# Kernel tuning notes

Measured on AMD Instinct MI355X. Metric: run time of the kernel, lower is better.

The kernel has to match this reference:

```python
import jax, jax.numpy as jnp
import numpy as np

N = 512
NODE_IN = 64
NODE_OUT = 64
ED_IN = 32
ED_OUT = 32
STATE = 80  # must satisfy 2*NODE_IN + ED_IN == 2*STATE
SLOPE = 0.1
EPS = 1e-5


def setup_inputs() -> dict:
    key = jax.random.key(0)
    ks = jax.random.split(key, 10)
    def lin(k, out_f, in_f):
        return jax.random.normal(k, (out_f, in_f), jnp.float32) / np.sqrt(in_f).astype(np.float32)
    x = jax.random.normal(ks[0], (N, NODE_IN), jnp.float32)
    edge_attr = jax.random.normal(ks[1], (N * N, ED_IN), jnp.float32)
    mask = jax.random.randint(ks[2], (N * N, 1), 0, 2).astype(jnp.int32)
    return {
        "x": x,
        "edge_attr": edge_attr,
        "mask": mask,
        "W_nu": lin(ks[3], NODE_OUT, NODE_IN),
        "b_nu": jnp.zeros((NODE_OUT,), jnp.float32),
        "W_h2": lin(ks[4], STATE, 2 * STATE),
        "b_h2": jnp.zeros((STATE,), jnp.float32),
        "W_eo": lin(ks[5], ED_OUT, STATE),
        "b_eo": jnp.zeros((ED_OUT,), jnp.float32),
        "e_vec": jax.random.normal(ks[6], (2 * NODE_OUT + ED_OUT,), jnp.float32) * 0.1,
        "bn_n_w": jnp.ones((NODE_OUT,), jnp.float32),
        "bn_n_b": jnp.zeros((NODE_OUT,), jnp.float32),
        "bn_e_w": jnp.ones((ED_OUT,), jnp.float32),
        "bn_e_b": jnp.zeros((ED_OUT,), jnp.float32),
    }


def _lrelu(v):
    return jax.nn.leaky_relu(v, SLOPE)


def _bn(v, w, b):
    # BatchNorm1d, training-mode (batch stats, biased variance)
    mu = v.mean(axis=0)
    var = v.var(axis=0)
    return (v - mu) / jnp.sqrt(var + EPS) * w + b


def reference(x, edge_attr, mask, W_nu, b_nu, W_h2, b_h2, W_eo, b_eo, e_vec,
              bn_n_w, bn_n_b, bn_e_w, bn_e_b):
    n = x.shape[0]
    m = mask.astype(x.dtype)  # [N*N, 1]
    # triplet_e[i*N+j] = [x_i, edge_attr_{ij}, x_j]
    src = jnp.repeat(x, n, axis=0)          # [N*N, NODE_IN]
    dst = jnp.tile(x, (n, 1))               # [N*N, NODE_IN]
    triplet_e = jnp.concatenate([src, edge_attr, dst], axis=-1)  # [N*N, 2*STATE]
    # NOTE: ed_trans_layer / ed_hidden_1 outputs are dead code in the source.
    h = _lrelu(triplet_e @ W_h2.T + b_h2)                 # [N*N, STATE]
    new_edge_attr = _lrelu(h @ W_eo.T + b_eo)             # [N*N, ED_OUT]
    new_edge_attr = new_edge_attr * m
    xn = _lrelu(x @ W_nu.T + b_nu)                        # [N, NODE_OUT]
    triplet_n = jnp.concatenate(
        [jnp.repeat(xn, n, axis=0), new_edge_attr, jnp.tile(xn, (n, 1))], axis=-1
    ).reshape(n, n, 2 * NODE_OUT + ED_OUT)
    scores = _lrelu(jnp.einsum("ijd,d->ij", triplet_n, e_vec))  # [N, N]
    att = jax.nn.softmax(scores, axis=1)
    att = (att.reshape(n * n, 1) * m).reshape(n, n)
    # dropout disabled (deterministic / eval)
    new_x = att @ xn                                       # [N, NODE_OUT]
    new_x = _bn(new_x, bn_n_w, bn_n_b)
    new_edge_attr = _bn(new_edge_attr, bn_e_w, bn_e_b)
    return new_x, new_edge_attr
```

## Files before the change

kernel.cpp:

```cpp
#include <hip/hip_runtime.h>

#define SLOPE 0.1f
#define EPS 1e-5f

typedef __bf16 bf16x8 __attribute__((ext_vector_type(8)));
typedef unsigned short u16x8 __attribute__((ext_vector_type(8)));
typedef float f32x4 __attribute__((ext_vector_type(4)));

#define WS_ESUM 0
#define WS_ESQ 32
#define WS_A 192
#define WS_B 704
#define WS_XN 1216
#define WS_NEWX 33984
#define WS_P1B 66752
#define WS_P2 107712
#define WS_SC 148672
#define WSH_WB 821632
#define WSH_WO 826752

__device__ __forceinline__ float lrelu(float v) { return v > 0.f ? v : SLOPE * v; }
__device__ __forceinline__ unsigned short f2bf(float f) {
  unsigned x = __float_as_uint(f);
  return (unsigned short)((x + 0x7fffu + ((x >> 16) & 1u)) >> 16);
}

__global__ void __launch_bounds__(256) k1(const float* __restrict__ x,
                                          const float* __restrict__ W_nu,
                                          const float* __restrict__ b_nu,
                                          const float* __restrict__ W_h2,
                                          const float* __restrict__ b_h2,
                                          const float* __restrict__ W_eo,
                                          const float* __restrict__ ev,
                                          float* ws, float* __restrict__ part) {
  int blk = blockIdx.x;
  int tid = threadIdx.x;
  unsigned short* wsh = (unsigned short*)ws;
  if (blk < 128) {
    __shared__ float wlds[64 * 65];
#pragma unroll
    for (int it = 0; it < 16; it++) {
      int idx = it * 256 + tid;
      wlds[(idx >> 6) * 65 + (idx & 63)] = W_nu[idx];
    }
    int gid = blk * 256 + tid;
    part[gid] = 0.f;
    if (gid < 5120) {
      wsh[WSH_WB + gid] = f2bf(W_h2[(gid >> 6) * 160 + 64 + (gid & 63)]);
    } else if (gid < 8192) {
      int idx = gid - 5120;
      int n = idx / 96, kk = idx - 96 * n;
      wsh[WSH_WO + idx] = (kk < 80) ? f2bf(W_eo[n * 80 + kk]) : (unsigned short)0;
    }
    __syncthreads();
    int i = blk * 4 + (tid >> 6);
    int c = tid & 63;
    float acc = b_nu[c];
    const float* xr = x + i * 64;
#pragma unroll 8
    for (int k = 0; k < 64; k++) acc += xr[k] * wlds[c * 65 + k];
    float xnv = lrelu(acc);
    ws[WS_XN + i * 64 + c] = xnv;
    float va = xnv * ev[c];
    float vb = xnv * ev[96 + c];
#pragma unroll
    for (int off = 32; off >= 1; off >>= 1) {
      va += __shfl_xor(va, off, 64);
      vb += __shfl_xor(vb, off, 64);
    }
    if (c == 0) { ws[WS_A + i] = va; ws[WS_B + i] = vb; }
  } else {
    int b2 = blk - 128;
    int bm = b2 & 7, bn = b2 >> 3;
    int wave = tid >> 6, lane = tid & 63;
    int c16 = lane & 15, q = lane >> 4;
    int n = bn * 16 + c16;
    const float* wrow = (n < 80) ? (W_h2 + n * 160) : (W_h2 + (n - 80) * 160 + 96);
    int mrow = bm * 64 + wave * 16 + c16;
    bf16x8 bf[2], af[2];
#pragma unroll
    for (int ks = 0; ks < 2; ks++) {
      const float* bs = wrow + ks * 32 + q * 8;
      const float* as = x + mrow * 64 + ks * 32 + q * 8;
      u16x8 ub, ua;
#pragma unroll
      for (int jj = 0; jj < 8; jj++) { ub[jj] = f2bf(bs[jj]); ua[jj] = f2bf(as[jj]); }
      bf[ks] = __builtin_bit_cast(bf16x8, ub);
      af[ks] = __builtin_bit_cast(bf16x8, ua);
    }
    float bias = (n < 80) ? b_h2[n] : 0.f;
    f32x4 acc = {bias, bias, bias, bias};
    acc = __builtin_amdgcn_mfma_f32_16x16x32_bf16(af[0], bf[0], acc, 0, 0, 0);
    acc = __builtin_amdgcn_mfma_f32_16x16x32_bf16(af[1], bf[1], acc, 0, 0, 0);
#pragma unroll
    for (int r = 0; r < 4; r++) {
      int mm = bm * 64 + wave * 16 + q * 4 + r;
      if (n < 80) ws[WS_P1B + mm * 80 + n] = acc[r];
      else        ws[WS_P2 + mm * 80 + (n - 80)] = acc[r];
    }
  }
}

__global__ void __launch_bounds__(256) k2(const float* __restrict__ ea,
                                          const int* __restrict__ mask,
                                          const float* __restrict__ b_eo,
                                          const float* __restrict__ ev,
                                          float* ws,
                                          float* __restrict__ part,
                                          float* __restrict__ out_e) {
  __shared__ unsigned short ht[64 * 104];
  __shared__ float wred[2][4][32];
  int tid = threadIdx.x;
  int wave = tid >> 6, lane = tid & 63;
  int c16 = lane & 15, q = lane >> 4;
  int blk = blockIdx.x;
  int i = blk >> 3, j0 = (blk & 7) << 6;
  const unsigned short* wsh = (const unsigned short*)ws;

  bf16x8 wb[5];
#pragma unroll
  for (int t = 0; t < 5; t++)
    wb[t] = __builtin_bit_cast(
        bf16x8, *(const u16x8*)(wsh + WSH_WB + (t * 16 + c16) * 64 + q * 8));
  int mA = i * 512 + j0 + wave * 16 + c16;
  bf16x8 af;
  {
    const float* src = ea + mA * 32 + q * 8;
    u16x8 u;
#pragma unroll
    for (int jj = 0; jj < 8; jj++) u[jj] = f2bf(src[jj]);
    af = __builtin_bit_cast(bf16x8, u);
  }

  f32x4 acc[5];
#pragma unroll
  for (int t = 0; t < 5; t++) {
    int n = t * 16 + c16;
    float p1v = ws[WS_P1B + i * 80 + n];
#pragma unroll
    for (int r = 0; r < 4; r++) {
      int j = j0 + wave * 16 + q * 4 + r;
      acc[t][r] = p1v + ws[WS_P2 + j * 80 + n];
    }
  }
#pragma unroll
  for (int t = 0; t < 5; t++)
    acc[t] = __builtin_amdgcn_mfma_f32_16x16x32_bf16(af, wb[t], acc[t], 0, 0, 0);

#pragma unroll
  for (int t = 0; t < 5; t++)
#pragma unroll
    for (int r = 0; r < 4; r++)
      ht[(wave * 16 + q * 4 + r) * 104 + t * 16 + c16] = f2bf(lrelu(acc[t][r]));

  bf16x8 wo[2][3];
#pragma unroll
  for (int t2 = 0; t2 < 2; t2++)
#pragma unroll
    for (int s = 0; s < 3; s++)
      wo[t2][s] = __builtin_bit_cast(
          bf16x8,
          *(const u16x8*)(wsh + WSH_WO + (t2 * 16 + c16) * 96 + s * 32 + q * 8));

  f32x4 z4 = {0.f, 0.f, 0.f, 0.f};
  f32x4 acc2[2] = {z4, z4};
  int hrow = wave * 16 + c16;
#pragma unroll
  for (int s = 0; s < 3; s++) {
    int kk = s * 32 + q * 8;
    u16x8 hbits = {0, 0, 0, 0, 0, 0, 0, 0};
    if (kk < 80) hbits = *(const u16x8*)&ht[hrow * 104 + kk];
    bf16x8 ha = __builtin_bit_cast(bf16x8, hbits);
#pragma unroll
    for (int t2 = 0; t2 < 2; t2++)
      acc2[t2] = __builtin_amdgcn_mfma_f32_16x16x32_bf16(ha, wo[t2][s], acc2[t2], 0, 0, 0);
  }

  float beo[2] = {b_eo[c16], b_eo[16 + c16]};
  float eve[2] = {ev[64 + c16], ev[80 + c16]};
  float ne[2][4];
  float scs[2] = {0.f, 0.f}, scss[2] = {0.f, 0.f};
#pragma unroll
  for (int t2 = 0; t2 < 2; t2++)
#pragma unroll
    for (int r = 0; r < 4; r++) {
      int m = i * 512 + j0 + wave * 16 + q * 4 + r;
      float mf = mask[m] ? 1.f : 0.f;
      float v = lrelu(acc2[t2][r] + beo[t2]) * mf;
      ne[t2][r] = v;
      scs[t2] += v;
      scss[t2] += v * v;
      out_e[m * 32 + t2 * 16 + c16] = v;
    }
#pragma unroll
  for (int t2 = 0; t2 < 2; t2++) {
    float a_ = scs[t2], b_ = scss[t2];
    a_ += __shfl_xor(a_, 16, 64); a_ += __shfl_xor(a_, 32, 64);
    b_ += __shfl_xor(b_, 16, 64); b_ += __shfl_xor(b_, 32, 64);
    if (q == 0) {
      wred[0][wave][t2 * 16 + c16] = a_;
      wred[1][wave][t2 * 16 + c16] = b_;
    }
  }
  float se[4];
#pragma unroll
  for (int r = 0; r < 4; r++) {
    float s = ne[0][r] * eve[0] + ne[1][r] * eve[1];
#pragma unroll
    for (int off = 8; off >= 1; off >>= 1) s += __shfl_xor(s, off, 64);
    se[r] = s;
  }
  if (c16 < 4) {
    float s = (c16 == 0) ? se[0] : (c16 == 1) ? se[1] : (c16 == 2) ? se[2] : se[3];
    int j = j0 + wave * 16 + q * 4 + c16;
    ws[WS_SC + i * 512 + j] = lrelu(ws[WS_A + i] + ws[WS_B + j] + s);
  }
  __syncthreads();
  if (tid < 64) {
    int half = tid >> 5;
    int col = tid & 31;
    float v = wred[half][0][col] + wred[half][1][col] + wred[half][2][col] +
              wred[half][3][col];
    atomicAdd(&part[(blk >> 3) * 64 + tid], v);
  }
}

__global__ void __launch_bounds__(512) k3(const int* __restrict__ mask,
                                          const float* __restrict__ part,
                                          float* ws) {
  __shared__ float att[512];
  __shared__ float red[8];
  __shared__ float nx[8][64];
  int i = blockIdx.x, tid = threadIdx.x;
  int wave = tid >> 6, lane = tid & 63;
  if (i == 512) {
    int c = tid & 63, g = tid >> 6;
    float a = 0.f;
    for (int s = g; s < 512; s += 8) a += part[s * 64 + c];
    nx[g][c] = a;
    __syncthreads();
    if (tid < 64) {
      float t = 0.f;
#pragma unroll
      for (int g2 = 0; g2 < 8; g2++) t += nx[g2][tid];
      ws[WS_ESUM + tid] = t;
    }
    return;
  }
  float p = __expf(ws[WS_SC + i * 512 + tid]);
  float sm = p;
#pragma unroll
  for (int off = 32; off >= 1; off >>= 1) sm += __shfl_xor(sm, off, 64);
  if (lane == 0) red[wave] = sm;
  __syncthreads();
  float tot = red[0] + red[1] + red[2] + red[3] + red[4] + red[5] + red[6] + red[7];
  att[tid] = p * (1.f / tot) * (mask[i * 512 + tid] ? 1.f : 0.f);
  __syncthreads();
  int c = lane;
  const float* xn = ws + WS_XN;
  float accv = 0.f;
#pragma unroll 4
  for (int u = 0; u < 64; u++) {
    int j = wave * 64 + u;
    accv += att[j] * xn[j * 64 + c];
  }
  nx[wave][c] = accv;
  __syncthreads();
  if (tid < 64) {
    float s = 0.f;
#pragma unroll
    for (int w = 0; w < 8; w++) s += nx[w][tid];
    ws[WS_NEWX + i * 64 + tid] = s;
  }
}

__global__ void __launch_bounds__(256) k5(const float* __restrict__ bn_n_w,
                                          const float* __restrict__ bn_n_b,
                                          const float* __restrict__ bn_e_w,
                                          const float* __restrict__ bn_e_b,
                                          const float* __restrict__ ws,
                                          float* __restrict__ out) {
  int blk = blockIdx.x, tid = threadIdx.x;
  if (blk < 8) {
    __shared__ float s1[4][64], s2[4][64], scl[64], sh[64];
    int c = tid & 63, g = tid >> 6;
    float a = 0.f, b = 0.f;
#pragma unroll 4
    for (int u = 0; u < 128; u++) {
      float v = ws[WS_NEWX + (g * 128 + u) * 64 + c];
      a += v;
      b += v * v;
    }
    s1[g][c] = a;
    s2[g][c] = b;
    __syncthreads();
    if (tid < 64) {
      float sum = s1[0][tid] + s1[1][tid] + s1[2][tid] + s1[3][tid];
      float ssq = s2[0][tid] + s2[1][tid] + s2[2][tid] + s2[3][tid];
      float mean = sum * (1.f / 512.f);
      float var = ssq * (1.f / 512.f) - mean * mean;
      float s = bn_n_w[tid] * rsqrtf(fmaxf(var, 0.f) + EPS);
      scl[tid] = s;
      sh[tid] = bn_n_b[tid] - mean * s;
    }
    __syncthreads();
#pragma unroll 4
    for (int u = 0; u < 16; u++) {
      int idx = blk * 4096 + u * 256 + tid;
      int c2 = idx & 63;
      out[idx] = ws[WS_NEWX + idx] * scl[c2] + sh[c2];
    }
  } else {
    __shared__ float esc[32], esh[32];
    if (tid < 32) {
      float mean = ws[WS_ESUM + tid] * (1.f / 262144.f);
      float var = ws[WS_ESQ + tid] * (1.f / 262144.f) - mean * mean;
      float s = bn_e_w[tid] * rsqrtf(fmaxf(var, 0.f) + EPS);
      esc[tid] = s;
      esh[tid] = bn_e_b[tid] - mean * s;
    }
    __syncthreads();
    float* oe = out + 32768;
    int base = ((blk - 8) * 256 + tid) * 8;
    f32x4 r0 = *(const f32x4*)(oe + base);
    f32x4 r1 = *(const f32x4*)(oe + base + 4);
    int c0 = base & 31;
    f32x4 w0, w1;
#pragma unroll
    for (int u = 0; u < 4; u++) {
      w0[u] = r0[u] * esc[c0 + u] + esh[c0 + u];
      w1[u] = r1[u] * esc[c0 + 4 + u] + esh[c0 + 4 + u];
    }
    *(f32x4*)(oe + base) = w0;
    *(f32x4*)(oe + base + 4) = w1;
  }
}

extern "C" void kernel_launch(void* const* d_in, const int* in_sizes, int n_in,
                              void* d_out, int out_size, void* d_ws, size_t ws_size,
                              hipStream_t stream) {
  const float* x = (const float*)d_in[0];
  const float* ea = (const float*)d_in[1];
  const int* mask = (const int*)d_in[2];
  const float* Wnu = (const float*)d_in[3];
  const float* bnu = (const float*)d_in[4];
  const float* Wh2 = (const float*)d_in[5];
  const float* bh2 = (const float*)d_in[6];
  const float* Weo = (const float*)d_in[7];
  const float* beo = (const float*)d_in[8];
  const float* ev = (const float*)d_in[9];
  const float* bnw = (const float*)d_in[10];
  const float* bnb = (const float*)d_in[11];
  const float* bew = (const float*)d_in[12];
  const float* beb = (const float*)d_in[13];
  float* ws = (float*)d_ws;
  float* out = (float*)d_out;
  float* part = out;

  k1<<<208, 256, 0, stream>>>(x, Wnu, bnu, Wh2, bh2, Weo, ev, ws, part);
  k2<<<4096, 256, 0, stream>>>(ea, mask, beo, ev, ws, part, out + 32768);
  k3<<<513, 512, 0, stream>>>(mask, part, ws);
  k5<<<4104, 256, 0, stream>>>(bnw, bnb, bew, beb, ws, out);
}
```

Before: 167.6 us.

## Fuse softmax/aggregation into edge kernel and stage edge output as bf16

The edge MLP kernel now runs one 512-thread block per source node i, looping over all 512 destinations. Scores stay in shared memory, so the softmax and att@xn aggregation happen in the same kernel instead of a separate pass. Per-row BN partial sums go to workspace with no atomics, and a single-block kernel finalises the edge BN scale and shift. The edge features are staged as packed bf16 in workspace and the final kernel converts and normalises them into the fp32 output, halving intermediate traffic. The cost is fewer blocks (512 vs 4096), less parallelism, and extra bf16 rounding before BN.

```diff
diff --git a/kernel.cpp b/kernel.cpp
--- a/kernel.cpp
+++ b/kernel.cpp
@@ -6,23 +6,28 @@
 typedef __bf16 bf16x8 __attribute__((ext_vector_type(8)));
 typedef unsigned short u16x8 __attribute__((ext_vector_type(8)));
 typedef float f32x4 __attribute__((ext_vector_type(4)));
-
-#define WS_ESUM 0
-#define WS_ESQ 32
-#define WS_A 192
-#define WS_B 704
-#define WS_XN 1216
-#define WS_NEWX 33984
-#define WS_P1B 66752
-#define WS_P2 107712
-#define WS_SC 148672
-#define WSH_WB 821632
-#define WSH_WO 826752
+typedef unsigned u32x4 __attribute__((ext_vector_type(4)));
+
+#define WS_ESC 0
+#define WS_ESH 32
+#define WS_A 64
+#define WS_B 576
+#define WS_XN 1088
+#define WS_NEWX 33856
+#define WS_P1B 66624
+#define WS_P2 107584
+#define WS_PART 148544
+#define WSH_WB 362624
+#define WSH_WO 367744
+#define WSH_NE 370816
 
 __device__ __forceinline__ float lrelu(float v) { return v > 0.f ? v : SLOPE * v; }
 __device__ __forceinline__ unsigned short f2bf(float f) {
   unsigned x = __float_as_uint(f);
   return (unsigned short)((x + 0x7fffu + ((x >> 16) & 1u)) >> 16);
+}
+__device__ __forceinline__ float bf2f(unsigned short u) {
+  return __uint_as_float(((unsigned)u) << 16);
 }
 
 __global__ void __launch_bounds__(256) k1(const float* __restrict__ x,
@@ -32,7 +37,7 @@
                                           const float* __restrict__ b_h2,
                                           const float* __restrict__ W_eo,
                                           const float* __restrict__ ev,
-                                          float* ws, float* __restrict__ part) {
+                                          float* ws) {
   int blk = blockIdx.x;
   int tid = threadIdx.x;
   unsigned short* wsh = (unsigned short*)ws;
@@ -44,7 +49,6 @@
       wlds[(idx >> 6) * 65 + (idx & 63)] = W_nu[idx];
     }
     int gid = blk * 256 + tid;
-    part[gid] = 0.f;
     if (gid < 5120) {
       wsh[WSH_WB + gid] = f2bf(W_h2[(gid >> 6) * 160 + 64 + (gid & 63)]);
     } else if (gid < 8192) {
@@ -77,7 +81,7 @@
     int n = bn * 16 + c16;
     const float* wrow = (n < 80) ? (W_h2 + n * 160) : (W_h2 + (n - 80) * 160 + 96);
     int mrow = bm * 64 + wave * 16 + c16;
-    bf16x8 bf[2], af[2];
+    bf16x8 bfr[2], afr[2];
 #pragma unroll
     for (int ks = 0; ks < 2; ks++) {
       const float* bs = wrow + ks * 32 + q * 8;
@@ -85,13 +89,13 @@
       u16x8 ub, ua;
 #pragma unroll
       for (int jj = 0; jj < 8; jj++) { ub[jj] = f2bf(bs[jj]); ua[jj] = f2bf(as[jj]); }
-      bf[ks] = __builtin_bit_cast(bf16x8, ub);
-      af[ks] = __builtin_bit_cast(bf16x8, ua);
+      bfr[ks] = __builtin_bit_cast(bf16x8, ub);
+      afr[ks] = __builtin_bit_cast(bf16x8, ua);
     }
     float bias = (n < 80) ? b_h2[n] : 0.f;
     f32x4 acc = {bias, bias, bias, bias};
-    acc = __builtin_amdgcn_mfma_f32_16x16x32_bf16(af[0], bf[0], acc, 0, 0, 0);
-    acc = __builtin_amdgcn_mfma_f32_16x16x32_bf16(af[1], bf[1], acc, 0, 0, 0);
+    acc = __builtin_amdgcn_mfma_f32_16x16x32_bf16(afr[0], bfr[0], acc, 0, 0, 0);
+    acc = __builtin_amdgcn_mfma_f32_16x16x32_bf16(afr[1], bfr[1], acc, 0, 0, 0);
 #pragma unroll
     for (int r = 0; r < 4; r++) {
       int mm = bm * 64 + wave * 16 + q * 4 + r;
@@ -101,58 +105,33 @@
   }
 }
 
-__global__ void __launch_bounds__(256) k2(const float* __restrict__ ea,
+__global__ void __launch_bounds__(512) k2(const float* __restrict__ ea,
                                           const int* __restrict__ mask,
                                           const float* __restrict__ b_eo,
                                           const float* __restrict__ ev,
-                                          float* ws,
-                                          float* __restrict__ part,
-                                          float* __restrict__ out_e) {
-  __shared__ unsigned short ht[64 * 104];
-  __shared__ float wred[2][4][32];
+                                          float* ws) {
+  __shared__ unsigned short ht[128 * 104];
+  __shared__ float srow[512];
+  __shared__ float mlds[512];
+  __shared__ float p1s[80];
+  __shared__ float wred[2][8][32];
+  __shared__ float nx[8][64];
+  __shared__ float red[8];
   int tid = threadIdx.x;
-  int wave = tid >> 6, lane = tid & 63;
+  int w = tid >> 6, lane = tid & 63;
   int c16 = lane & 15, q = lane >> 4;
-  int blk = blockIdx.x;
-  int i = blk >> 3, j0 = (blk & 7) << 6;
+  int i = blockIdx.x;
   const unsigned short* wsh = (const unsigned short*)ws;
+  unsigned* ne32 = (unsigned*)((unsigned short*)ws + WSH_NE);
+
+  mlds[tid] = mask[i * 512 + tid] ? 1.f : 0.f;
+  if (tid < 80) p1s[tid] = ws[WS_P1B + i * 80 + tid];
 
   bf16x8 wb[5];
 #pragma unroll
   for (int t = 0; t < 5; t++)
     wb[t] = __builtin_bit_cast(
         bf16x8, *(const u16x8*)(wsh + WSH_WB + (t * 16 + c16) * 64 + q * 8));
-  int mA = i * 512 + j0 + wave * 16 + c16;
-  bf16x8 af;
-  {
-    const float* src = ea + mA * 32 + q * 8;
-    u16x8 u;
-#pragma unroll
-    for (int jj = 0; jj < 8; jj++) u[jj] = f2bf(src[jj]);
-    af = __builtin_bit_cast(bf16x8, u);
-  }
-
-  f32x4 acc[5];
-#pragma unroll
-  for (int t = 0; t < 5; t++) {
-    int n = t * 16 + c16;
-    float p1v = ws[WS_P1B + i * 80 + n];
-#pragma unroll
-    for (int r = 0; r < 4; r++) {
-      int j = j0 + wave * 16 + q * 4 + r;
-      acc[t][r] = p1v + ws[WS_P2 + j * 80 + n];
-    }
-  }
-#pragma unroll
-  for (int t = 0; t < 5; t++)
-    acc[t] = __builtin_amdgcn_mfma_f32_16x16x32_bf16(af, wb[t], acc[t], 0, 0, 0);
-
-#pragma unroll
-  for (int t = 0; t < 5; t++)
-#pragma unroll
-    for (int r = 0; r < 4; r++)
-      ht[(wave * 16 + q * 4 + r) * 104 + t * 16 + c16] = f2bf(lrelu(acc[t][r]));
-
   bf16x8 wo[2][3];
 #pragma unroll
   for (int t2 = 0; t2 < 2; t2++)
@@ -161,123 +140,141 @@
       wo[t2][s] = __builtin_bit_cast(
           bf16x8,
           *(const u16x8*)(wsh + WSH_WO + (t2 * 16 + c16) * 96 + s * 32 + q * 8));
-
-  f32x4 z4 = {0.f, 0.f, 0.f, 0.f};
-  f32x4 acc2[2] = {z4, z4};
-  int hrow = wave * 16 + c16;
-#pragma unroll
-  for (int s = 0; s < 3; s++) {
-    int kk = s * 32 + q * 8;
-    u16x8 hbits = {0, 0, 0, 0, 0, 0, 0, 0};
-    if (kk < 80) hbits = *(const u16x8*)&ht[hrow * 104 + kk];
-    bf16x8 ha = __builtin_bit_cast(bf16x8, hbits);
-#pragma unroll
-    for (int t2 = 0; t2 < 2; t2++)
-      acc2[t2] = __builtin_amdgcn_mfma_f32_16x16x32_bf16(ha, wo[t2][s], acc2[t2], 0, 0, 0);
-  }
-
-  float beo[2] = {b_eo[c16], b_eo[16 + c16]};
-  float eve[2] = {ev[64 + c16], ev[80 + c16]};
-  float ne[2][4];
-  float scs[2] = {0.f, 0.f}, scss[2] = {0.f, 0.f};
-#pragma unroll
-  for (int t2 = 0; t2 < 2; t2++)
+  float beo0 = b_eo[c16], beo1 = b_eo[16 + c16];
+  float eve0 = ev[64 + c16], eve1 = ev[80 + c16];
+  float a_i = ws[WS_A + i];
+  __syncthreads();
+
+  float scs0 = 0.f, scss0 = 0.f, scs1 = 0.f, scss1 = 0.f;
+#pragma unroll 1
+  for (int mt = 0; mt < 4; mt++) {
+    int jb = w * 64 + mt * 16;
+    bf16x8 af;
+    {
+      const float* src = ea + (i * 512 + jb + c16) * 32 + q * 8;
+      u16x8 u;
+#pragma unroll
+      for (int jj = 0; jj < 8; jj++) u[jj] = f2bf(src[jj]);
+      af = __builtin_bit_cast(bf16x8, u);
+    }
+    f32x4 acc[5];
+#pragma unroll
+    for (int t = 0; t < 5; t++) {
+      int n = t * 16 + c16;
+      float p1v = p1s[n];
+#pragma unroll
+      for (int r = 0; r < 4; r++)
+        acc[t][r] = p1v + ws[WS_P2 + (jb + q * 4 + r) * 80 + n];
+    }
+#pragma unroll
+    for (int t = 0; t < 5; t++)
+      acc[t] = __builtin_amdgcn_mfma_f32_16x16x32_bf16(af, wb[t], acc[t], 0, 0, 0);
+#pragma unroll
+    for (int t = 0; t < 5; t++)
+#pragma unroll
+      for (int r = 0; r < 4; r++)
+        ht[(w * 16 + q * 4 + r) * 104 + t * 16 + c16] = f2bf(lrelu(acc[t][r]));
+    f32x4 acc2[2] = {{0.f, 0.f, 0.f, 0.f}, {0.f, 0.f, 0.f, 0.f}};
+    int hrow = w * 16 + c16;
+#pragma unroll
+    for (int s = 0; s < 3; s++) {
+      int kk = s * 32 + q * 8;
+      u16x8 hb = {0, 0, 0, 0, 0, 0, 0, 0};
+      if (kk < 80) hb = *(const u16x8*)&ht[hrow * 104 + kk];
+      bf16x8 ha = __builtin_bit_cast(bf16x8, hb);
+      acc2[0] = __builtin_amdgcn_mfma_f32_16x16x32_bf16(ha, wo[0][s], acc2[0], 0, 0, 0);
+      acc2[1] = __builtin_amdgcn_mfma_f32_16x16x32_bf16(ha, wo[1][s], acc2[1], 0, 0, 0);
+    }
+    float se[4];
 #pragma unroll
     for (int r = 0; r < 4; r++) {
-      int m = i * 512 + j0 + wave * 16 + q * 4 + r;
-      float mf = mask[m] ? 1.f : 0.f;
-      float v = lrelu(acc2[t2][r] + beo[t2]) * mf;
-      ne[t2][r] = v;
-      scs[t2] += v;
-      scss[t2] += v * v;
-      out_e[m * 32 + t2 * 16 + c16] = v;
-    }
-#pragma unroll
-  for (int t2 = 0; t2 < 2; t2++) {
-    float a_ = scs[t2], b_ = scss[t2];
-    a_ += __shfl_xor(a_, 16, 64); a_ += __shfl_xor(a_, 32, 64);
-    b_ += __shfl_xor(b_, 16, 64); b_ += __shfl_xor(b_, 32, 64);
-    if (q == 0) {
-      wred[0][wave][t2 * 16 + c16] = a_;
-      wred[1][wave][t2 * 16 + c16] = b_;
-    }
-  }
-  float se[4];
-#pragma unroll
-  for (int r = 0; r < 4; r++) {
-    float s = ne[0][r] * eve[0] + ne[1][r] * eve[1];
-#pragma unroll
-    for (int off = 8; off >= 1; off >>= 1) s += __shfl_xor(s, off, 64);
-    se[r] = s;
-  }
-  if (c16 < 4) {
-    float s = (c16 == 0) ? se[0] : (c16 == 1) ? se[1] : (c16 == 2) ? se[2] : se[3];
-    int j = j0 + wave * 16 + q * 4 + c16;
-    ws[WS_SC + i * 512 + j] = lrelu(ws[WS_A + i] + ws[WS_B + j] + s);
+      int jl = jb + q * 4 + r;
+      float mf = mlds[jl];
+      float v0 = lrelu(acc2[0][r] + beo0) * mf;
+      float v1 = lrelu(acc2[1][r] + beo1) * mf;
+      scs0 += v0; scss0 += v0 * v0;
+      scs1 += v1; scss1 += v1 * v1;
+      ne32[(i * 512 + jl) * 16 + c16] =
+          (unsigned)f2bf(v0) | ((unsigned)f2bf(v1) << 16);
+      float s = v0 * eve0 + v1 * eve1;
+#pragma unroll
+      for (int off = 8; off >= 1; off >>= 1) s += __shfl_xor(s, off, 64);
+      se[r] = s;
+    }
+    if (c16 < 4) {
+      int jl = jb + q * 4 + c16;
+      float s = (c16 == 0) ? se[0] : (c16 == 1) ? se[1] : (c16 == 2) ? se[2] : se[3];
+      srow[jl] = lrelu(a_i + ws[WS_B + jl] + s);
+    }
+  }
+  scs0 += __shfl_xor(scs0, 16, 64); scs0 += __shfl_xor(scs0, 32, 64);
+  scss0 += __shfl_xor(scss0, 16, 64); scss0 += __shfl_xor(scss0, 32, 64);
+  scs1 += __shfl_xor(scs1, 16, 64); scs1 += __shfl_xor(scs1, 32, 64);
+  scss1 += __shfl_xor(scss1, 16, 64); scss1 += __shfl_xor(scss1, 32, 64);
+  if (q == 0) {
+    wred[0][w][c16] = scs0; wred[0][w][16 + c16] = scs1;
+    wred[1][w][c16] = scss0; wred[1][w][16 + c16] = scss1;
   }
   __syncthreads();
   if (tid < 64) {
-    int half = tid >> 5;
-    int col = tid & 31;
-    float v = wred[half][0][col] + wred[half][1][col] + wred[half][2][col] +
-              wred[half][3][col];
-    atomicAdd(&part[(blk >> 3) * 64 + tid], v);
-  }
-}
-
-__global__ void __launch_bounds__(512) k3(const int* __restrict__ mask,
-                                          const float* __restrict__ part,
-                                          float* ws) {
-  __shared__ float att[512];
-  __shared__ float red[8];
-  __shared__ float nx[8][64];
-  int i = blockIdx.x, tid = threadIdx.x;
-  int wave = tid >> 6, lane = tid & 63;
-  if (i == 512) {
-    int c = tid & 63, g = tid >> 6;
-    float a = 0.f;
-    for (int s = g; s < 512; s += 8) a += part[s * 64 + c];
-    nx[g][c] = a;
-    __syncthreads();
-    if (tid < 64) {
-      float t = 0.f;
-#pragma unroll
-      for (int g2 = 0; g2 < 8; g2++) t += nx[g2][tid];
-      ws[WS_ESUM + tid] = t;
-    }
-    return;
-  }
-  float p = __expf(ws[WS_SC + i * 512 + tid]);
+    int half = tid >> 5, col = tid & 31;
+    float v = 0.f;
+#pragma unroll
+    for (int ww = 0; ww < 8; ww++) v += wred[half][ww][col];
+    ws[WS_PART + i * 64 + tid] = v;
+  }
+  float p = __expf(srow[tid]);
   float sm = p;
 #pragma unroll
   for (int off = 32; off >= 1; off >>= 1) sm += __shfl_xor(sm, off, 64);
-  if (lane == 0) red[wave] = sm;
+  if (lane == 0) red[w] = sm;
   __syncthreads();
   float tot = red[0] + red[1] + red[2] + red[3] + red[4] + red[5] + red[6] + red[7];
-  att[tid] = p * (1.f / tot) * (mask[i * 512 + tid] ? 1.f : 0.f);
-  __syncthreads();
-  int c = lane;
-  const float* xn = ws + WS_XN;
+  srow[tid] = p * (1.f / tot) * mlds[tid];
   float accv = 0.f;
 #pragma unroll 4
   for (int u = 0; u < 64; u++) {
-    int j = wave * 64 + u;
-    accv += att[j] * xn[j * 64 + c];
-  }
-  nx[wave][c] = accv;
+    int j = w * 64 + u;
+    accv += srow[j] * ws[WS_XN + j * 64 + lane];
+  }
+  nx[w][lane] = accv;
   __syncthreads();
   if (tid < 64) {
     float s = 0.f;
 #pragma unroll
-    for (int w = 0; w < 8; w++) s += nx[w][tid];
+    for (int ww = 0; ww < 8; ww++) s += nx[ww][tid];
     ws[WS_NEWX + i * 64 + tid] = s;
+  }
+}
+
+__global__ void __launch_bounds__(512) k3(const float* __restrict__ bn_e_w,
+                                          const float* __restrict__ bn_e_b,
+                                          float* ws) {
+  __shared__ float nx[8][64];
+  int tid = threadIdx.x;
+  int g = tid >> 6, c = tid & 63;
+  float a = 0.f;
+  for (int s = g; s < 512; s += 8) a += ws[WS_PART + s * 64 + c];
+  nx[g][c] = a;
+  __syncthreads();
+  if (tid < 64) {
+    float t = 0.f;
+#pragma unroll
+    for (int g2 = 0; g2 < 8; g2++) t += nx[g2][tid];
+    nx[0][tid] = t;
+  }
+  __syncthreads();
+  if (tid < 32) {
+    float mean = nx[0][tid] * (1.f / 262144.f);
+    float var = nx[0][tid + 32] * (1.f / 262144.f) - mean * mean;
+    float s = bn_e_w[tid] * rsqrtf(fmaxf(var, 0.f) + EPS);
+    ws[WS_ESC + tid] = s;
+    ws[WS_ESH + tid] = bn_e_b[tid] - mean * s;
   }
 }
 
 __global__ void __launch_bounds__(256) k5(const float* __restrict__ bn_n_w,
                                           const float* __restrict__ bn_n_b,
-                                          const float* __restrict__ bn_e_w,
-                                          const float* __restrict__ bn_e_b,
                                           const float* __restrict__ ws,
                                           float* __restrict__ out) {
   int blk = blockIdx.x, tid = threadIdx.x;
@@ -311,28 +308,24 @@
       out[idx] = ws[WS_NEWX + idx] * scl[c2] + sh[c2];
     }
   } else {
-    __shared__ float esc[32], esh[32];
-    if (tid < 32) {
-      float mean = ws[WS_ESUM + tid] * (1.f / 262144.f);
-      float var = ws[WS_ESQ + tid] * (1.f / 262144.f) - mean * mean;
-      float s = bn_e_w[tid] * rsqrtf(fmaxf(var, 0.f) + EPS);
-      esc[tid] = s;
-      esh[tid] = bn_e_b[tid] - mean * s;
-    }
-    __syncthreads();
+    const unsigned* ne32 = (const unsigned*)((const unsigned short*)ws + WSH_NE);
+    int b4 = ((blk - 8) * 256 + tid) * 4;
+    u32x4 raw = *(const u32x4*)(ne32 + b4);
+    int e32 = (b4 >> 4) * 32;
+    int cb = b4 & 15;
+    f32x4 esc0 = *(const f32x4*)(ws + WS_ESC + cb);
+    f32x4 esc1 = *(const f32x4*)(ws + WS_ESC + 16 + cb);
+    f32x4 esh0 = *(const f32x4*)(ws + WS_ESH + cb);
+    f32x4 esh1 = *(const f32x4*)(ws + WS_ESH + 16 + cb);
+    f32x4 lo, hi;
+#pragma unroll
+    for (int u = 0; u < 4; u++) {
+      lo[u] = bf2f((unsigned short)(raw[u] & 0xffffu)) * esc0[u] + esh0[u];
+      hi[u] = bf2f((unsigned short)(raw[u] >> 16)) * esc1[u] + esh1[u];
+    }
     float* oe = out + 32768;
-    int base = ((blk - 8) * 256 + tid) * 8;
-    f32x4 r0 = *(const f32x4*)(oe + base);
-    f32x4 r1 = *(const f32x4*)(oe + base + 4);
-    int c0 = base & 31;
-    f32x4 w0, w1;
-#pragma unroll
-    for (int u = 0; u < 4; u++) {
-      w0[u] = r0[u] * esc[c0 + u] + esh[c0 + u];
-      w1[u] = r1[u] * esc[c0 + 4 + u] + esh[c0 + 4 + u];
-    }
-    *(f32x4*)(oe + base) = w0;
-    *(f32x4*)(oe + base + 4) = w1;
+    *(f32x4*)(oe + e32 + cb) = lo;
+    *(f32x4*)(oe + e32 + 16 + cb) = hi;
   }
 }
 
@@ -355,10 +348,9 @@
   const float* beb = (const float*)d_in[13];
   float* ws = (float*)d_ws;
   float* out = (float*)d_out;
-  float* part = out;
-
-  k1<<<208, 256, 0, stream>>>(x, Wnu, bnu, Wh2, bh2, Weo, ev, ws, part);
-  k2<<<4096, 256, 0, stream>>>(ea, mask, beo, ev, ws, part, out + 32768);
-  k3<<<513, 512, 0, stream>>>(mask, part, ws);
-  k5<<<4104, 256, 0, stream>>>(bnw, bnb, bew, beb, ws, out);
-}
+
+  k1<<<208, 256, 0, stream>>>(x, Wnu, bnu, Wh2, bh2, Weo, ev, ws);
+  k2<<<512, 512, 0, stream>>>(ea, mask, beo, ev, ws);
+  k3<<<1, 512, 0, stream>>>(bew, beb, ws);
+  k5<<<4104, 256, 0, stream>>>(bnw, bnb, ws, out);
+}
```

New measurement: 170.7 us. Within noise of the previous version (+1.8%).
